# Kernel optimization log

Measured on AMD Instinct MI355X. Metric: run time of the kernel, lower is better.

The kernel has to match this reference:

```python
import jax, jax.numpy as jnp
import numpy as np

N, F, E = 65536, 64, 16   # batch, fields, embedding_size
H1, H2 = 8, 4             # hidden_dims
BN_EPS = 1e-5


def setup_inputs() -> dict:
    key = jax.random.key(0)
    ks = jax.random.split(key, 12)
    rn = lambda k, shape, sc=1.0: jax.random.normal(k, shape, dtype=jnp.float32) * sc
    return {
        "Xa": rn(ks[0], (N, F)),
        "Xc": rn(ks[1], (N, F)),
        # per-field Linear(1,1) weights/biases (two first-order embedding lists)
        "w1": rn(ks[2], (F,)), "b1": rn(ks[3], (F,)),
        "w2": rn(ks[4], (F,)), "b2": rn(ks[5], (F,)),
        # per-field Linear(1,E) weights/biases (two second-order embedding lists)
        "W1": rn(ks[6], (F, E)), "B1": rn(ks[7], (F, E)),
        "W2": rn(ks[8], (F, E)), "B2": rn(ks[9], (F, E)),
        # deep MLP: linear_1 (F*E -> 8) + BN, linear_2 (8 -> 4). No final layer (init bug).
        "lin1_w": rn(ks[10], (H1, F * E), 0.01), "lin1_b": jnp.zeros((H1,), jnp.float32),
        "bn1_gamma": jnp.ones((H1,), jnp.float32), "bn1_beta": jnp.zeros((H1,), jnp.float32),
        "lin2_w": rn(ks[11], (H2, H1), 0.01), "lin2_b": jnp.full((H2,), 0.21, jnp.float32),
    }


def reference(Xa, Xc, w1, b1, w2, b2, W1, B1, W2, B2,
              lin1_w, lin1_b, bn1_gamma, bn1_beta, lin2_w, lin2_b):
    n = Xa.shape[0]
    # ---- FM first order (faithful to the torch broadcast: arr_2[i] is (N,N)
    # with entry [r,c] = Xa[r,i]*(w2[i]*Xc[c,i]+b2[i]); only mean over the
    # concat dim is consumed, so compute the column-mean analytically). ----
    first1 = (w1 * Xa + b1) * Xc                         # (N,F)
    xc_mean = jnp.mean(Xc, axis=0)                       # (F,)
    first2_cmean = Xa * (w2 * xc_mean + b2)              # (N,F) = mean over c of arr_2
    fm_first_mean = jnp.mean(first1 + first2_cmean, axis=1, keepdims=True)  # (N,1)

    # ---- FM second order: per-field (N,E) embeddings, fully batched. ----
    Xa3 = Xa[:, :, None]                                 # (N,F,1)
    Xc3 = Xc[:, :, None]
    emb = (Xa3 * W1 + B1) * Xc3 + Xa3 * (W2 * Xc3 + B2)  # (N,F,E)
    s = emb.sum(axis=1)                                  # (N,E)
    fm_second = 0.5 * (s * s - (emb * emb).sum(axis=1))  # (N,E)
    fm_second_mean = jnp.mean(fm_second, axis=1, keepdims=True)  # (N,1)

    # ---- deep part: cat of per-field (N,E) -> (N, F*E), field-major. ----
    deep = emb.reshape(n, F * E)
    h = deep @ lin1_w.T + lin1_b                         # (N,8)
    mu = h.mean(axis=0)
    var = h.var(axis=0)                                  # biased, as BN training mode
    h = (h - mu) / jnp.sqrt(var + BN_EPS) * bn1_gamma + bn1_beta
    h = jnp.tanh(h)                                      # dropout = identity (eval)
    h = h @ lin2_w.T + lin2_b                            # (N,4) — no final projection (init bug)
    deep_mean = h.mean(axis=1, keepdims=True)            # (N,1)

    return fm_first_mean + fm_second_mean + deep_mean    # (N,1)
```

## Files before the change

kernel.cpp:

```cpp
#include <hip/hip_runtime.h>
#include <math.h>

#define NROWS 65536
#define BN_EPS 1e-5f
#define NBLK   1024

#define OFF_PARTIAL 0
#define OFF_H       65536
#define OFF_REC     589824
#define OFF_BLKT    595200
#define OFF_T       677120

__global__ __launch_bounds__(64) void precompute_kernel(
    const float* __restrict__ W1, const float* __restrict__ B1,
    const float* __restrict__ W2, const float* __restrict__ B2,
    const float* __restrict__ lin1_w, const float* __restrict__ w1,
    const float* __restrict__ b1, const float* __restrict__ b2,
    float* __restrict__ rec)
{
    int f = blockIdx.x, t = threadIdx.x;
    __shared__ float u[16], x[16], y[16];
    if (t < 16) {
        float uu = W1[f * 16 + t] + W2[f * 16 + t];
        float xx = B1[f * 16 + t];
        float yy = B2[f * 16 + t];
        u[t] = uu; x[t] = xx; y[t] = yy;
        rec[f * 84 + t]      = uu;
        rec[f * 84 + 16 + t] = xx;
        rec[f * 84 + 32 + t] = yy;
    }
    __syncthreads();
    if (t < 24) {
        int j = t & 7, which = t >> 3;
        const float* src = (which == 0) ? u : (which == 1) ? x : y;
        const float* lw = lin1_w + j * 1024 + f * 16;
        float acc = 0.f;
#pragma unroll
        for (int e = 0; e < 16; e++) acc = fmaf(src[e], lw[e], acc);
        rec[f * 84 + 48 + which * 8 + j] = acc;
    } else if (t < 30) {
        int q = t - 24;
        const float* s1 = (q == 0 || q == 3 || q == 4) ? u : (q == 1 || q == 5) ? x : y;
        const float* s2 = (q == 0) ? u : (q == 1 || q == 3) ? x : y;
        float acc = 0.f;
#pragma unroll
        for (int e = 0; e < 16; e++) acc = fmaf(s1[e], s2[e], acc);
        rec[f * 84 + 72 + q] = (q < 3 ? 1.f : 2.f) * acc;
    } else if (t == 30) {
        rec[f * 84 + 78] = w1[f];
        rec[f * 84 + 79] = b1[f];
        rec[f * 84 + 80] = b2[f];
        rec[f * 84 + 81] = 0.f;
        rec[f * 84 + 82] = 0.f;
        rec[f * 84 + 83] = 0.f;
    }
}

__global__ __launch_bounds__(256)
__attribute__((amdgpu_waves_per_eu(2, 4)))
void main_kernel(
    const float* __restrict__ Xa, const float* __restrict__ Xc,
    const float* __restrict__ rec, const float* __restrict__ lin1_b,
    float* __restrict__ ws_partial, float* __restrict__ ws_h,
    float* __restrict__ ws_blkT)
{
    __shared__ __align__(16) float smem[7424];

    int tid  = threadIdx.x;
    int lane = tid & 63;
    int wv   = tid >> 6;
    int wu   = __builtin_amdgcn_readfirstlane(wv);
    int blk  = blockIdx.x;
    int f0   = wu * 16;
    int row  = blk * 64 + lane;

    {
        const float4* src = (const float4*)rec;
        float4* dst = (float4*)smem;
        for (int i = tid; i < 1344; i += 256) dst[i] = src[i];
    }

    const float4* pa = (const float4*)(Xa + (size_t)row * 64 + f0);
    const float4* pc = (const float4*)(Xc + (size_t)row * 64 + f0);
    float a_[16], c_[16];
#pragma unroll
    for (int k = 0; k < 4; k++) {
        float4 av = pa[k], cv = pc[k];
        a_[k * 4] = av.x; a_[k * 4 + 1] = av.y; a_[k * 4 + 2] = av.z; a_[k * 4 + 3] = av.w;
        c_[k * 4] = cv.x; c_[k * 4 + 1] = cv.y; c_[k * 4 + 2] = cv.z; c_[k * 4 + 3] = cv.w;
    }
    __syncthreads();

    float s[16], hh[8];
#pragma unroll
    for (int e = 0; e < 16; e++) s[e] = 0.f;
#pragma unroll
    for (int j = 0; j < 8; j++) hh[j] = 0.f;
    float p1 = 0.f, p2a = 0.f, qsum = 0.f;

    const float* recw = smem + f0 * 84;
#pragma unroll 1
    for (int i = 0; i < 16; i++) {
        const float* r = recw + i * 84;
        float a = a_[i], c = c_[i];
        float pp = a * c;
        p1  = fmaf(fmaf(r[78], a, r[79]), c, p1);
        p2a = fmaf(a, r[80], p2a);
        qsum = fmaf(pp * pp, r[72], qsum);
        qsum = fmaf(c * c,   r[73], qsum);
        qsum = fmaf(a * a,   r[74], qsum);
        qsum = fmaf(pp * c,  r[75], qsum);
        qsum = fmaf(pp * a,  r[76], qsum);
        qsum = fmaf(pp,      r[77], qsum);
#pragma unroll
        for (int e = 0; e < 16; e++)
            s[e] = fmaf(pp, r[e], fmaf(c, r[16 + e], fmaf(a, r[32 + e], s[e])));
#pragma unroll
        for (int j = 0; j < 8; j++)
            hh[j] = fmaf(pp, r[48 + j], fmaf(c, r[56 + j], fmaf(a, r[64 + j], hh[j])));
    }

    {
        float cs[16];
#pragma unroll
        for (int i = 0; i < 16; i++) cs[i] = c_[i];
#pragma unroll
        for (int off = 1; off < 64; off <<= 1) {
#pragma unroll
            for (int i = 0; i < 16; i++) cs[i] += __shfl_xor(cs[i], off);
        }
        if (lane == 0) {
#pragma unroll
            for (int i = 0; i < 16; i++)
                ws_blkT[(size_t)(f0 + i) * NBLK + blk] = cs[i];
        }
    }

    __syncthreads();
    {
        float* cmb = smem + (wv * 64 + lane) * 29;
#pragma unroll
        for (int e = 0; e < 16; e++) cmb[e] = s[e];
#pragma unroll
        for (int j = 0; j < 8; j++) cmb[16 + j] = hh[j];
        cmb[24] = p1;
        cmb[25] = p2a;
        cmb[26] = qsum;
    }
    __syncthreads();

    if (tid < 64) {
        float S[16], H[8], P1 = 0.f, P2 = 0.f, Q = 0.f;
#pragma unroll
        for (int e = 0; e < 16; e++) S[e] = 0.f;
#pragma unroll
        for (int j = 0; j < 8; j++) H[j] = 0.f;
#pragma unroll
        for (int w = 0; w < 4; w++) {
            const float* c2 = smem + (w * 64 + tid) * 29;
#pragma unroll
            for (int e = 0; e < 16; e++) S[e] += c2[e];
#pragma unroll
            for (int j = 0; j < 8; j++) H[j] += c2[16 + j];
            P1 += c2[24];
            P2 += c2[25];
            Q  += c2[26];
        }
#pragma unroll
        for (int j = 0; j < 8; j++) H[j] += lin1_b[j];

        float ss = 0.f;
#pragma unroll
        for (int e = 0; e < 16; e++) ss = fmaf(S[e], S[e], ss);
        int rr = blk * 64 + tid;
        ws_partial[rr] = (P1 + P2) * (1.f / 64.f) + (ss - Q) * (0.5f / 16.f);
        *(float4*)(ws_h + (size_t)rr * 8)     = make_float4(H[0], H[1], H[2], H[3]);
        *(float4*)(ws_h + (size_t)rr * 8 + 4) = make_float4(H[4], H[5], H[6], H[7]);

        float bn[16];
#pragma unroll
        for (int j = 0; j < 8; j++) { bn[j] = H[j]; bn[8 + j] = H[j] * H[j]; }
#pragma unroll
        for (int off = 1; off < 64; off <<= 1) {
#pragma unroll
            for (int i = 0; i < 16; i++) bn[i] += __shfl_xor(bn[i], off);
        }
        if (tid == 0) {
#pragma unroll
            for (int i = 0; i < 16; i++)
                ws_blkT[(size_t)(64 + i) * NBLK + blk] = bn[i];
        }
    }
}

__global__ __launch_bounds__(256) void reduce_kernel(
    const float* __restrict__ ws_blkT, float* __restrict__ T)
{
    int gtid = blockIdx.x * 256 + threadIdx.x;
    int v = gtid >> 6;
    int lane = gtid & 63;
    const float* p = ws_blkT + (size_t)v * NBLK + lane;
    float acc = 0.f;
#pragma unroll
    for (int k = 0; k < 16; k++) acc += p[k * 64];
#pragma unroll
    for (int off = 32; off; off >>= 1) acc += __shfl_xor(acc, off);
    if (lane == 0) T[v] = acc;
}

__global__ __launch_bounds__(256) void final_kernel(
    const float* __restrict__ Xa, const float* __restrict__ w2,
    const float* __restrict__ gamma, const float* __restrict__ beta,
    const float* __restrict__ lin2_w, const float* __restrict__ lin2_b,
    const float* __restrict__ T, const float* __restrict__ ws_partial,
    const float* __restrict__ ws_h, float* __restrict__ out)
{
    __shared__ float sg[64], sScale[8], sShift[8], sColw[8];
    __shared__ float sBsum;
    int tid = threadIdx.x;
    if (tid < 64) {
        sg[tid] = w2[tid] * (T[tid] * (1.f / 65536.f));
    } else if (tid < 72) {
        int j = tid - 64;
        float mu  = T[64 + j] * (1.f / 65536.f);
        float var = T[72 + j] * (1.f / 65536.f) - mu * mu;
        float sc = gamma[j] / sqrtf(var + BN_EPS);
        sScale[j] = sc;
        sShift[j] = beta[j] - mu * sc;
    } else if (tid < 80) {
        int j = tid - 72;
        sColw[j] = lin2_w[j] + lin2_w[8 + j] + lin2_w[16 + j] + lin2_w[24 + j];
    } else if (tid == 80) {
        sBsum = lin2_b[0] + lin2_b[1] + lin2_b[2] + lin2_b[3];
    }
    __syncthreads();

    int row  = (blockIdx.x * 256 + tid) >> 1;
    int half = tid & 1;
    int fo   = half * 32;

    const float4* xa4 = (const float4*)(Xa + (size_t)row * 64 + fo);
    float p2b = 0.f;
#pragma unroll
    for (int k = 0; k < 8; k++) {
        float4 vv = xa4[k];
        int b = fo + k * 4;
        p2b += vv.x * sg[b] + vv.y * sg[b + 1] + vv.z * sg[b + 2] + vv.w * sg[b + 3];
    }

    float4 hq = *(const float4*)(ws_h + (size_t)row * 8 + half * 4);
    float hv[4] = {hq.x, hq.y, hq.z, hq.w};
    float dmp = 0.f;
#pragma unroll
    for (int jj = 0; jj < 4; jj++) {
        int j = half * 4 + jj;
        float hn = tanhf(hv[jj] * sScale[j] + sShift[j]);
        dmp = fmaf(hn, sColw[j], dmp);
    }

    float val = p2b * (1.f / 64.f) + dmp * 0.25f;
    val += __shfl_xor(val, 1);
    if (!half)
        out[row] = val + ws_partial[row] + sBsum * 0.25f;
}

extern "C" void kernel_launch(void* const* d_in, const int* in_sizes, int n_in,
                              void* d_out, int out_size, void* d_ws, size_t ws_size,
                              hipStream_t stream) {
    const float* Xa        = (const float*)d_in[0];
    const float* Xc        = (const float*)d_in[1];
    const float* w1        = (const float*)d_in[2];
    const float* b1        = (const float*)d_in[3];
    const float* w2        = (const float*)d_in[4];
    const float* b2        = (const float*)d_in[5];
    const float* W1        = (const float*)d_in[6];
    const float* B1        = (const float*)d_in[7];
    const float* W2        = (const float*)d_in[8];
    const float* B2        = (const float*)d_in[9];
    const float* lin1_w    = (const float*)d_in[10];
    const float* lin1_b    = (const float*)d_in[11];
    const float* bn1_gamma = (const float*)d_in[12];
    const float* bn1_beta  = (const float*)d_in[13];
    const float* lin2_w    = (const float*)d_in[14];
    const float* lin2_b    = (const float*)d_in[15];

    float* ws  = (float*)d_ws;
    float* out = (float*)d_out;

    float* ws_partial = ws + OFF_PARTIAL;
    float* ws_h       = ws + OFF_H;
    float* ws_rec     = ws + OFF_REC;
    float* ws_blkT    = ws + OFF_BLKT;
    float* ws_T       = ws + OFF_T;

    precompute_kernel<<<64, 64, 0, stream>>>(W1, B1, W2, B2, lin1_w,
                                             w1, b1, b2, ws_rec);
    main_kernel<<<NBLK, 256, 0, stream>>>(Xa, Xc, ws_rec, lin1_b,
                                          ws_partial, ws_h, ws_blkT);
    reduce_kernel<<<20, 256, 0, stream>>>(ws_blkT, ws_T);
    final_kernel<<<512, 256, 0, stream>>>(Xa, w2, bn1_gamma, bn1_beta,
                                          lin2_w, lin2_b, ws_T,
                                          ws_partial, ws_h, out);
}
```

Before: 128.9 us.

## Process two rows per thread in main kernel to reuse shared-memory weights

Each thread now computes two rows (row and row+64), so every weight value read from shared memory serves two rows' FMAs. The grid is halved to 512 blocks and the shared-memory combine buffer is doubled. The column-sum partials per block are merged, and the reduce kernel's loop counts are adjusted to match. This cuts LDS read traffic and per-block overhead, at the cost of higher register pressure, more LDS per block and fewer blocks to fill the GPU.

```diff
diff --git a/kernel.cpp b/kernel.cpp
--- a/kernel.cpp
+++ b/kernel.cpp
@@ -3,7 +3,8 @@
 
 #define NROWS 65536
 #define BN_EPS 1e-5f
-#define NBLK   1024
+#define MBLK   512
+#define TSTR   1024
 
 #define OFF_PARTIAL 0
 #define OFF_H       65536
@@ -64,7 +65,7 @@
     float* __restrict__ ws_partial, float* __restrict__ ws_h,
     float* __restrict__ ws_blkT)
 {
-    __shared__ __align__(16) float smem[7424];
+    __shared__ __align__(16) float smem[14848];
 
     int tid  = threadIdx.x;
     int lane = tid & 63;
@@ -72,7 +73,8 @@
     int wu   = __builtin_amdgcn_readfirstlane(wv);
     int blk  = blockIdx.x;
     int f0   = wu * 16;
-    int row  = blk * 64 + lane;
+    int row0 = blk * 128 + lane;
+    int row1 = row0 + 64;
 
     {
         const float4* src = (const float4*)rec;
@@ -80,50 +82,76 @@
         for (int i = tid; i < 1344; i += 256) dst[i] = src[i];
     }
 
-    const float4* pa = (const float4*)(Xa + (size_t)row * 64 + f0);
-    const float4* pc = (const float4*)(Xc + (size_t)row * 64 + f0);
-    float a_[16], c_[16];
+    const float4* pa0 = (const float4*)(Xa + (size_t)row0 * 64 + f0);
+    const float4* pc0 = (const float4*)(Xc + (size_t)row0 * 64 + f0);
+    const float4* pa1 = (const float4*)(Xa + (size_t)row1 * 64 + f0);
+    const float4* pc1 = (const float4*)(Xc + (size_t)row1 * 64 + f0);
+    float a_[16], c_[16], a2_[16], c2_[16];
 #pragma unroll
     for (int k = 0; k < 4; k++) {
-        float4 av = pa[k], cv = pc[k];
+        float4 av = pa0[k], cv = pc0[k];
         a_[k * 4] = av.x; a_[k * 4 + 1] = av.y; a_[k * 4 + 2] = av.z; a_[k * 4 + 3] = av.w;
         c_[k * 4] = cv.x; c_[k * 4 + 1] = cv.y; c_[k * 4 + 2] = cv.z; c_[k * 4 + 3] = cv.w;
-    }
-    __syncthreads();
-
-    float s[16], hh[8];
-#pragma unroll
-    for (int e = 0; e < 16; e++) s[e] = 0.f;
-#pragma unroll
-    for (int j = 0; j < 8; j++) hh[j] = 0.f;
-    float p1 = 0.f, p2a = 0.f, qsum = 0.f;
+        float4 av2 = pa1[k], cv2 = pc1[k];
+        a2_[k * 4] = av2.x; a2_[k * 4 + 1] = av2.y; a2_[k * 4 + 2] = av2.z; a2_[k * 4 + 3] = av2.w;
+        c2_[k * 4] = cv2.x; c2_[k * 4 + 1] = cv2.y; c2_[k * 4 + 2] = cv2.z; c2_[k * 4 + 3] = cv2.w;
+    }
+    __syncthreads();
+
+    float s[16], s2[16], hh[8], hh2[8];
+#pragma unroll
+    for (int e = 0; e < 16; e++) { s[e] = 0.f; s2[e] = 0.f; }
+#pragma unroll
+    for (int j = 0; j < 8; j++) { hh[j] = 0.f; hh2[j] = 0.f; }
+    float p1_0 = 0.f, p2a_0 = 0.f, q_0 = 0.f;
+    float p1_1 = 0.f, p2a_1 = 0.f, q_1 = 0.f;
 
     const float* recw = smem + f0 * 84;
 #pragma unroll 1
     for (int i = 0; i < 16; i++) {
         const float* r = recw + i * 84;
-        float a = a_[i], c = c_[i];
-        float pp = a * c;
-        p1  = fmaf(fmaf(r[78], a, r[79]), c, p1);
-        p2a = fmaf(a, r[80], p2a);
-        qsum = fmaf(pp * pp, r[72], qsum);
-        qsum = fmaf(c * c,   r[73], qsum);
-        qsum = fmaf(a * a,   r[74], qsum);
-        qsum = fmaf(pp * c,  r[75], qsum);
-        qsum = fmaf(pp * a,  r[76], qsum);
-        qsum = fmaf(pp,      r[77], qsum);
-#pragma unroll
-        for (int e = 0; e < 16; e++)
-            s[e] = fmaf(pp, r[e], fmaf(c, r[16 + e], fmaf(a, r[32 + e], s[e])));
-#pragma unroll
-        for (int j = 0; j < 8; j++)
-            hh[j] = fmaf(pp, r[48 + j], fmaf(c, r[56 + j], fmaf(a, r[64 + j], hh[j])));
+        float a0 = a_[i],  c0 = c_[i];
+        float a1 = a2_[i], c1 = c2_[i];
+        float pp0 = a0 * c0, pp1 = a1 * c1;
+
+        float rw1 = r[78], rb1 = r[79], rb2 = r[80];
+        p1_0  = fmaf(fmaf(rw1, a0, rb1), c0, p1_0);
+        p1_1  = fmaf(fmaf(rw1, a1, rb1), c1, p1_1);
+        p2a_0 = fmaf(a0, rb2, p2a_0);
+        p2a_1 = fmaf(a1, rb2, p2a_1);
+
+        float q0 = r[72], q1 = r[73], q2 = r[74], q3 = r[75], q4 = r[76], q5 = r[77];
+        q_0 = fmaf(pp0 * pp0, q0, q_0);
+        q_0 = fmaf(c0 * c0,   q1, q_0);
+        q_0 = fmaf(a0 * a0,   q2, q_0);
+        q_0 = fmaf(pp0 * c0,  q3, q_0);
+        q_0 = fmaf(pp0 * a0,  q4, q_0);
+        q_0 = fmaf(pp0,       q5, q_0);
+        q_1 = fmaf(pp1 * pp1, q0, q_1);
+        q_1 = fmaf(c1 * c1,   q1, q_1);
+        q_1 = fmaf(a1 * a1,   q2, q_1);
+        q_1 = fmaf(pp1 * c1,  q3, q_1);
+        q_1 = fmaf(pp1 * a1,  q4, q_1);
+        q_1 = fmaf(pp1,       q5, q_1);
+
+#pragma unroll
+        for (int e = 0; e < 16; e++) {
+            float u = r[e], x = r[16 + e], y = r[32 + e];
+            s[e]  = fmaf(pp0, u, fmaf(c0, x, fmaf(a0, y, s[e])));
+            s2[e] = fmaf(pp1, u, fmaf(c1, x, fmaf(a1, y, s2[e])));
+        }
+#pragma unroll
+        for (int j = 0; j < 8; j++) {
+            float w1c = r[48 + j], w2c = r[56 + j], w3c = r[64 + j];
+            hh[j]  = fmaf(pp0, w1c, fmaf(c0, w2c, fmaf(a0, w3c, hh[j])));
+            hh2[j] = fmaf(pp1, w1c, fmaf(c1, w2c, fmaf(a1, w3c, hh2[j])));
+        }
     }
 
     {
         float cs[16];
 #pragma unroll
-        for (int i = 0; i < 16; i++) cs[i] = c_[i];
+        for (int i = 0; i < 16; i++) cs[i] = c_[i] + c2_[i];
 #pragma unroll
         for (int off = 1; off < 64; off <<= 1) {
 #pragma unroll
@@ -132,24 +160,28 @@
         if (lane == 0) {
 #pragma unroll
             for (int i = 0; i < 16; i++)
-                ws_blkT[(size_t)(f0 + i) * NBLK + blk] = cs[i];
+                ws_blkT[(size_t)(f0 + i) * TSTR + blk] = cs[i];
         }
     }
 
     __syncthreads();
     {
-        float* cmb = smem + (wv * 64 + lane) * 29;
-#pragma unroll
-        for (int e = 0; e < 16; e++) cmb[e] = s[e];
-#pragma unroll
-        for (int j = 0; j < 8; j++) cmb[16 + j] = hh[j];
-        cmb[24] = p1;
-        cmb[25] = p2a;
-        cmb[26] = qsum;
-    }
-    __syncthreads();
-
-    if (tid < 64) {
+        float* cmb0 = smem + (wv * 64 + lane) * 29;
+        float* cmb1 = smem + 7424 + (wv * 64 + lane) * 29;
+#pragma unroll
+        for (int e = 0; e < 16; e++) { cmb0[e] = s[e]; cmb1[e] = s2[e]; }
+#pragma unroll
+        for (int j = 0; j < 8; j++) { cmb0[16 + j] = hh[j]; cmb1[16 + j] = hh2[j]; }
+        cmb0[24] = p1_0;  cmb1[24] = p1_1;
+        cmb0[25] = p2a_0; cmb1[25] = p2a_1;
+        cmb0[26] = q_0;   cmb1[26] = q_1;
+    }
+    __syncthreads();
+
+    if (tid < 128) {
+        int set = tid >> 6;
+        int l   = tid & 63;
+        const float* base = smem + set * 7424;
         float S[16], H[8], P1 = 0.f, P2 = 0.f, Q = 0.f;
 #pragma unroll
         for (int e = 0; e < 16; e++) S[e] = 0.f;
@@ -157,7 +189,7 @@
         for (int j = 0; j < 8; j++) H[j] = 0.f;
 #pragma unroll
         for (int w = 0; w < 4; w++) {
-            const float* c2 = smem + (w * 64 + tid) * 29;
+            const float* c2 = base + (w * 64 + l) * 29;
 #pragma unroll
             for (int e = 0; e < 16; e++) S[e] += c2[e];
 #pragma unroll
@@ -172,7 +204,7 @@
         float ss = 0.f;
 #pragma unroll
         for (int e = 0; e < 16; e++) ss = fmaf(S[e], S[e], ss);
-        int rr = blk * 64 + tid;
+        int rr = blk * 128 + set * 64 + l;
         ws_partial[rr] = (P1 + P2) * (1.f / 64.f) + (ss - Q) * (0.5f / 16.f);
         *(float4*)(ws_h + (size_t)rr * 8)     = make_float4(H[0], H[1], H[2], H[3]);
         *(float4*)(ws_h + (size_t)rr * 8 + 4) = make_float4(H[4], H[5], H[6], H[7]);
@@ -185,10 +217,10 @@
 #pragma unroll
             for (int i = 0; i < 16; i++) bn[i] += __shfl_xor(bn[i], off);
         }
-        if (tid == 0) {
+        if (l == 0) {
 #pragma unroll
             for (int i = 0; i < 16; i++)
-                ws_blkT[(size_t)(64 + i) * NBLK + blk] = bn[i];
+                ws_blkT[(size_t)(64 + i) * TSTR + blk * 2 + set] = bn[i];
         }
     }
 }
@@ -199,10 +231,15 @@
     int gtid = blockIdx.x * 256 + threadIdx.x;
     int v = gtid >> 6;
     int lane = gtid & 63;
-    const float* p = ws_blkT + (size_t)v * NBLK + lane;
+    const float* p = ws_blkT + (size_t)v * TSTR + lane;
     float acc = 0.f;
-#pragma unroll
-    for (int k = 0; k < 16; k++) acc += p[k * 64];
+    if (v < 64) {
+#pragma unroll
+        for (int k = 0; k < 8; k++) acc += p[k * 64];
+    } else {
+#pragma unroll
+        for (int k = 0; k < 16; k++) acc += p[k * 64];
+    }
 #pragma unroll
     for (int off = 32; off; off >>= 1) acc += __shfl_xor(acc, off);
     if (lane == 0) T[v] = acc;
@@ -295,7 +332,7 @@
 
     precompute_kernel<<<64, 64, 0, stream>>>(W1, B1, W2, B2, lin1_w,
                                              w1, b1, b2, ws_rec);
-    main_kernel<<<NBLK, 256, 0, stream>>>(Xa, Xc, ws_rec, lin1_b,
+    main_kernel<<<MBLK, 256, 0, stream>>>(Xa, Xc, ws_rec, lin1_b,
                                           ws_partial, ws_h, ws_blkT);
     reduce_kernel<<<20, 256, 0, stream>>>(ws_blkT, ws_T);
     final_kernel<<<512, 256, 0, stream>>>(Xa, w2, bn1_gamma, bn1_beta,
```

Result: faster. 124.2 us (-3.7%).

## Process four row sets per thread to reuse LDS coefficient loads across rows

Applied to the files above, without the earlier changes.

Each block now handles 256 rows instead of 64, with every thread computing four rows. Per-field coefficients are loaded from LDS into registers once and reused across the four row sets, which cuts LDS traffic per FMA. The grid drops to 256 blocks, so only one block per CU on a 256-CU part, and the register and LDS footprint grows (occupancy hint lowered, 116KB LDS). The reduction kernel is adjusted for the new partial-sum layout.

```diff
diff --git a/kernel.cpp b/kernel.cpp
--- a/kernel.cpp
+++ b/kernel.cpp
@@ -3,7 +3,8 @@
 
 #define NROWS 65536
 #define BN_EPS 1e-5f
-#define NBLK   1024
+#define MBLK   256
+#define TSTR   1024
 
 #define OFF_PARTIAL 0
 #define OFF_H       65536
@@ -57,14 +58,14 @@
 }
 
 __global__ __launch_bounds__(256)
-__attribute__((amdgpu_waves_per_eu(2, 4)))
+__attribute__((amdgpu_waves_per_eu(1, 2)))
 void main_kernel(
     const float* __restrict__ Xa, const float* __restrict__ Xc,
     const float* __restrict__ rec, const float* __restrict__ lin1_b,
     float* __restrict__ ws_partial, float* __restrict__ ws_h,
     float* __restrict__ ws_blkT)
 {
-    __shared__ __align__(16) float smem[7424];
+    __shared__ __align__(16) float smem[29696];
 
     int tid  = threadIdx.x;
     int lane = tid & 63;
@@ -72,7 +73,7 @@
     int wu   = __builtin_amdgcn_readfirstlane(wv);
     int blk  = blockIdx.x;
     int f0   = wu * 16;
-    int row  = blk * 64 + lane;
+    int row0 = blk * 256 + lane;
 
     {
         const float4* src = (const float4*)rec;
@@ -80,50 +81,71 @@
         for (int i = tid; i < 1344; i += 256) dst[i] = src[i];
     }
 
-    const float4* pa = (const float4*)(Xa + (size_t)row * 64 + f0);
-    const float4* pc = (const float4*)(Xc + (size_t)row * 64 + f0);
-    float a_[16], c_[16];
-#pragma unroll
-    for (int k = 0; k < 4; k++) {
-        float4 av = pa[k], cv = pc[k];
-        a_[k * 4] = av.x; a_[k * 4 + 1] = av.y; a_[k * 4 + 2] = av.z; a_[k * 4 + 3] = av.w;
-        c_[k * 4] = cv.x; c_[k * 4 + 1] = cv.y; c_[k * 4 + 2] = cv.z; c_[k * 4 + 3] = cv.w;
-    }
-    __syncthreads();
-
-    float s[16], hh[8];
-#pragma unroll
-    for (int e = 0; e < 16; e++) s[e] = 0.f;
-#pragma unroll
-    for (int j = 0; j < 8; j++) hh[j] = 0.f;
-    float p1 = 0.f, p2a = 0.f, qsum = 0.f;
+    float a_[4][16], c_[4][16];
+#pragma unroll
+    for (int st = 0; st < 4; st++) {
+        const float4* pa = (const float4*)(Xa + (size_t)(row0 + st * 64) * 64 + f0);
+        const float4* pc = (const float4*)(Xc + (size_t)(row0 + st * 64) * 64 + f0);
+#pragma unroll
+        for (int k = 0; k < 4; k++) {
+            float4 av = pa[k], cv = pc[k];
+            a_[st][k * 4] = av.x; a_[st][k * 4 + 1] = av.y;
+            a_[st][k * 4 + 2] = av.z; a_[st][k * 4 + 3] = av.w;
+            c_[st][k * 4] = cv.x; c_[st][k * 4 + 1] = cv.y;
+            c_[st][k * 4 + 2] = cv.z; c_[st][k * 4 + 3] = cv.w;
+        }
+    }
+    __syncthreads();
+
+    float s_[4][16], hh_[4][8];
+    float p1_[4], p2a_[4], q_[4];
+#pragma unroll
+    for (int st = 0; st < 4; st++) {
+#pragma unroll
+        for (int e = 0; e < 16; e++) s_[st][e] = 0.f;
+#pragma unroll
+        for (int j = 0; j < 8; j++) hh_[st][j] = 0.f;
+        p1_[st] = 0.f; p2a_[st] = 0.f; q_[st] = 0.f;
+    }
 
     const float* recw = smem + f0 * 84;
 #pragma unroll 1
     for (int i = 0; i < 16; i++) {
         const float* r = recw + i * 84;
-        float a = a_[i], c = c_[i];
-        float pp = a * c;
-        p1  = fmaf(fmaf(r[78], a, r[79]), c, p1);
-        p2a = fmaf(a, r[80], p2a);
-        qsum = fmaf(pp * pp, r[72], qsum);
-        qsum = fmaf(c * c,   r[73], qsum);
-        qsum = fmaf(a * a,   r[74], qsum);
-        qsum = fmaf(pp * c,  r[75], qsum);
-        qsum = fmaf(pp * a,  r[76], qsum);
-        qsum = fmaf(pp,      r[77], qsum);
-#pragma unroll
-        for (int e = 0; e < 16; e++)
-            s[e] = fmaf(pp, r[e], fmaf(c, r[16 + e], fmaf(a, r[32 + e], s[e])));
-#pragma unroll
-        for (int j = 0; j < 8; j++)
-            hh[j] = fmaf(pp, r[48 + j], fmaf(c, r[56 + j], fmaf(a, r[64 + j], hh[j])));
+        float ru[16], rx[16], ry[16], rA1[8], rA2[8], rA3[8];
+#pragma unroll
+        for (int e = 0; e < 16; e++) { ru[e] = r[e]; rx[e] = r[16 + e]; ry[e] = r[32 + e]; }
+#pragma unroll
+        for (int j = 0; j < 8; j++) { rA1[j] = r[48 + j]; rA2[j] = r[56 + j]; rA3[j] = r[64 + j]; }
+        float q0 = r[72], q1 = r[73], q2 = r[74], q3 = r[75], q4 = r[76], q5 = r[77];
+        float rw1 = r[78], rb1 = r[79], rb2 = r[80];
+
+#pragma unroll
+        for (int st = 0; st < 4; st++) {
+            float a = a_[st][i], c = c_[st][i];
+            float pp = a * c;
+            p1_[st]  = fmaf(fmaf(rw1, a, rb1), c, p1_[st]);
+            p2a_[st] = fmaf(a, rb2, p2a_[st]);
+            q_[st] = fmaf(pp * pp, q0, q_[st]);
+            q_[st] = fmaf(c * c,   q1, q_[st]);
+            q_[st] = fmaf(a * a,   q2, q_[st]);
+            q_[st] = fmaf(pp * c,  q3, q_[st]);
+            q_[st] = fmaf(pp * a,  q4, q_[st]);
+            q_[st] = fmaf(pp,      q5, q_[st]);
+#pragma unroll
+            for (int e = 0; e < 16; e++)
+                s_[st][e] = fmaf(pp, ru[e], fmaf(c, rx[e], fmaf(a, ry[e], s_[st][e])));
+#pragma unroll
+            for (int j = 0; j < 8; j++)
+                hh_[st][j] = fmaf(pp, rA1[j], fmaf(c, rA2[j], fmaf(a, rA3[j], hh_[st][j])));
+        }
     }
 
     {
         float cs[16];
 #pragma unroll
-        for (int i = 0; i < 16; i++) cs[i] = c_[i];
+        for (int i = 0; i < 16; i++)
+            cs[i] = c_[0][i] + c_[1][i] + c_[2][i] + c_[3][i];
 #pragma unroll
         for (int off = 1; off < 64; off <<= 1) {
 #pragma unroll
@@ -132,24 +154,28 @@
         if (lane == 0) {
 #pragma unroll
             for (int i = 0; i < 16; i++)
-                ws_blkT[(size_t)(f0 + i) * NBLK + blk] = cs[i];
-        }
-    }
-
-    __syncthreads();
+                ws_blkT[(size_t)(f0 + i) * TSTR + blk] = cs[i];
+        }
+    }
+
+    __syncthreads();
+#pragma unroll
+    for (int st = 0; st < 4; st++) {
+        float* cmb = smem + st * 7424 + (wv * 64 + lane) * 29;
+#pragma unroll
+        for (int e = 0; e < 16; e++) cmb[e] = s_[st][e];
+#pragma unroll
+        for (int j = 0; j < 8; j++) cmb[16 + j] = hh_[st][j];
+        cmb[24] = p1_[st];
+        cmb[25] = p2a_[st];
+        cmb[26] = q_[st];
+    }
+    __syncthreads();
+
     {
-        float* cmb = smem + (wv * 64 + lane) * 29;
-#pragma unroll
-        for (int e = 0; e < 16; e++) cmb[e] = s[e];
-#pragma unroll
-        for (int j = 0; j < 8; j++) cmb[16 + j] = hh[j];
-        cmb[24] = p1;
-        cmb[25] = p2a;
-        cmb[26] = qsum;
-    }
-    __syncthreads();
-
-    if (tid < 64) {
+        int set = tid >> 6;
+        int l   = tid & 63;
+        const float* base = smem + set * 7424;
         float S[16], H[8], P1 = 0.f, P2 = 0.f, Q = 0.f;
 #pragma unroll
         for (int e = 0; e < 16; e++) S[e] = 0.f;
@@ -157,7 +183,7 @@
         for (int j = 0; j < 8; j++) H[j] = 0.f;
 #pragma unroll
         for (int w = 0; w < 4; w++) {
-            const float* c2 = smem + (w * 64 + tid) * 29;
+            const float* c2 = base + (w * 64 + l) * 29;
 #pragma unroll
             for (int e = 0; e < 16; e++) S[e] += c2[e];
 #pragma unroll
@@ -172,7 +198,7 @@
         float ss = 0.f;
 #pragma unroll
         for (int e = 0; e < 16; e++) ss = fmaf(S[e], S[e], ss);
-        int rr = blk * 64 + tid;
+        int rr = blk * 256 + set * 64 + l;
         ws_partial[rr] = (P1 + P2) * (1.f / 64.f) + (ss - Q) * (0.5f / 16.f);
         *(float4*)(ws_h + (size_t)rr * 8)     = make_float4(H[0], H[1], H[2], H[3]);
         *(float4*)(ws_h + (size_t)rr * 8 + 4) = make_float4(H[4], H[5], H[6], H[7]);
@@ -185,10 +211,10 @@
 #pragma unroll
             for (int i = 0; i < 16; i++) bn[i] += __shfl_xor(bn[i], off);
         }
-        if (tid == 0) {
+        if (l == 0) {
 #pragma unroll
             for (int i = 0; i < 16; i++)
-                ws_blkT[(size_t)(64 + i) * NBLK + blk] = bn[i];
+                ws_blkT[(size_t)(64 + i) * TSTR + blk * 4 + set] = bn[i];
         }
     }
 }
@@ -199,10 +225,15 @@
     int gtid = blockIdx.x * 256 + threadIdx.x;
     int v = gtid >> 6;
     int lane = gtid & 63;
-    const float* p = ws_blkT + (size_t)v * NBLK + lane;
+    const float* p = ws_blkT + (size_t)v * TSTR + lane;
     float acc = 0.f;
-#pragma unroll
-    for (int k = 0; k < 16; k++) acc += p[k * 64];
+    if (v < 64) {
+#pragma unroll
+        for (int k = 0; k < 4; k++) acc += p[k * 64];
+    } else {
+#pragma unroll
+        for (int k = 0; k < 16; k++) acc += p[k * 64];
+    }
 #pragma unroll
     for (int off = 32; off; off >>= 1) acc += __shfl_xor(acc, off);
     if (lane == 0) T[v] = acc;
@@ -295,7 +326,7 @@
 
     precompute_kernel<<<64, 64, 0, stream>>>(W1, B1, W2, B2, lin1_w,
                                              w1, b1, b2, ws_rec);
-    main_kernel<<<NBLK, 256, 0, stream>>>(Xa, Xc, ws_rec, lin1_b,
+    main_kernel<<<MBLK, 256, 0, stream>>>(Xa, Xc, ws_rec, lin1_b,
                                           ws_partial, ws_h, ws_blkT);
     reduce_kernel<<<20, 256, 0, stream>>>(ws_blkT, ws_T);
     final_kernel<<<512, 256, 0, stream>>>(Xa, w2, bn1_gamma, bn1_beta,
```

After: 147.3 us. 1.14x slower.
